# Kernel optimization log

Measured on AMD Instinct MI355X. Metric: run time of the kernel, lower is better.

## Reference

```python
import jax, jax.numpy as jnp
import numpy as np

L, H, DH = 4, 8, 64            # num_layers, num_heads, hidden_dim (= dim_per_head)
HD = H * DH                    # 512 = per-layer q/k/v width
R, BLOCK, NREG, NW = 3, 128, 8, 8   # n_hashes, block_size, num_regions, num_w_per_dist
CDIM, LAT = 2, 3               # coords_dim, latent_dim
SCALE = 1.0 / float(np.sqrt(DH))


def layer_norm(x, g, b):
    m = x.mean(-1, keepdims=True)
    v = ((x - m) ** 2).mean(-1, keepdims=True)
    return (x - m) * jax.lax.rsqrt(v + 1e-5) * g + b


def hept_attention(q, k, v, coords, batch, w_head, hash_proj):
    # HEPT: E2LSH hash + region/batch bucketing -> sort -> blockwise attention
    # with RPE distance bias, combined over hash rounds by logsumexp weights.
    N = q.shape[0]
    nb = N // BLOCK
    qh = q.reshape(N, H, DH)
    kh = k.reshape(N, H, DH)
    vh = v.reshape(N, H, DH)
    c0 = coords[:, 0]
    region = jnp.clip(((c0 - c0.min()) / (c0.max() - c0.min() + 1e-6) * NREG).astype(jnp.int32), 0, NREG - 1)
    c_rpe = coords[:, 1:]                       # [N, CDIM-1] dims used for RPE distances
    bf = batch.astype(jnp.float32)
    outs, lses = [], []
    for r in range(R):
        hv = coords @ hash_proj[r]              # [N] LSH projection
        hn = (hv - hv.min()) / (hv.max() - hv.min() + 1e-6)
        skey = (bf * NREG + region.astype(jnp.float32)) * 2.0 + hn  # batch-major, region, hash
        idx = jnp.argsort(skey)
        inv = jnp.argsort(idx)
        qs = qh[idx].reshape(nb, BLOCK, H, DH)
        ks = kh[idx].reshape(nb, BLOCK, H, DH)
        vs = vh[idx].reshape(nb, BLOCK, H, DH)
        cs = c_rpe[idx].reshape(nb, BLOCK, CDIM - 1)
        bs = batch[idx].reshape(nb, BLOCK)
        scores = jnp.einsum('bihd,bjhd->bhij', qs, ks) * SCALE     # [nb,H,B,B]
        d2 = (cs[:, :, None, :] - cs[:, None, :, :]) ** 2          # [nb,B,B,CDIM-1]
        scores = scores - jnp.einsum('hc,bijc->bhij', w_head, d2)  # RPE distance penalty
        scores = jnp.where((bs[:, :, None] == bs[:, None, :])[:, None], scores, -1e9)
        lse = jax.nn.logsumexp(scores, axis=-1)                    # [nb,H,B]
        p = jnp.exp(scores - lse[..., None])
        o = jnp.einsum('bhij,bjhd->bihd', p, vs).reshape(N, H, DH)
        outs.append(o[inv])
        lses.append(jnp.transpose(lse, (0, 2, 1)).reshape(N, H)[inv])
    wts = jax.nn.softmax(jnp.stack(lses), axis=0)[..., None]       # [R,N,H,1]
    return (wts * jnp.stack(outs)).sum(0).reshape(N, HD)


def _forward(x, coords, batch, enc_W1, enc_b1, enc_W2, enc_b2, ln1_g, ln1_b, wq, wk, wv,
             rpe_W, wo, ln2_g, ln2_b, ff_W1, ff_b1, ff_W2, ff_b2, W_cat,
             mlp_W1, mlp_b1, mlp_W2, mlp_b2, beta_W1, beta_b1, beta_W2, beta_b2,
             coord_W1, coord_b1, coord_W2, coord_b2, hash_proj):
    h0 = jax.nn.relu(x @ enc_W1 + enc_b1) @ enc_W2 + enc_b2
    feats = [h0]
    cur = h0
    for l in range(L):
        xn = layer_norm(cur, ln1_g[l], ln1_b[l])
        q = xn @ wq[l]
        k = xn @ wk[l]
        v = xn @ wv[l]
        # per-head positive RPE weights derived from w_rpe weight matrix
        w_head = jax.nn.softplus(rpe_W[l].reshape(CDIM - 1, NW, H, DH).mean(axis=(1, 3)).T)  # [H,CDIM-1]
        a = hept_attention(q, k, v, coords, batch, w_head, hash_proj) @ wo[l]
        cur = cur + a
        ffo = jax.nn.relu(layer_norm(cur, ln2_g[l], ln2_b[l]) @ ff_W1[l] + ff_b1[l]) @ ff_W2[l] + ff_b2[l]
        cur = cur + ffo
        feats.append(cur)
    enc2 = jnp.concatenate(feats, axis=-1) @ W_cat
    out = enc2 + (jax.nn.relu(enc2 @ mlp_W1 + mlp_b1) @ mlp_W2 + mlp_b2)
    eps = 1e-6
    beta = jnp.clip(jax.nn.sigmoid(jax.nn.relu(out @ beta_W1 + beta_b1) @ beta_W2 + beta_b2), eps, 1.0 - eps)
    hcoord = jax.nn.relu(out @ coord_W1 + coord_b1) @ coord_W2 + coord_b2
    return beta, hcoord


def setup_inputs() -> dict:
    key = jax.random.key(0)
    ks = jax.random.split(key, 40)
    N, IN_DIM = 32768, 16
    def w(i, shape, s=0.05):
        return jax.random.normal(ks[i], shape, jnp.float32) * s
    return dict(
        x=jax.random.normal(ks[0], (N, IN_DIM), jnp.float32),
        coords=jax.random.normal(ks[1], (N, CDIM), jnp.float32),
        batch=jnp.sort(jax.random.randint(ks[2], (N,), 0, 8)),
        enc_W1=w(3, (IN_DIM, DH)), enc_b1=jnp.zeros((DH,), jnp.float32),
        enc_W2=w(4, (DH, DH)), enc_b2=jnp.zeros((DH,), jnp.float32),
        ln1_g=jnp.ones((L, DH), jnp.float32), ln1_b=jnp.zeros((L, DH), jnp.float32),
        wq=w(5, (L, DH, HD)), wk=w(6, (L, DH, HD)), wv=w(7, (L, DH, HD)),
        rpe_W=w(8, (L, NW * (CDIM - 1), HD)),
        wo=w(9, (L, HD, DH)),
        ln2_g=jnp.ones((L, DH), jnp.float32), ln2_b=jnp.zeros((L, DH), jnp.float32),
        ff_W1=w(10, (L, DH, DH)), ff_b1=jnp.zeros((L, DH), jnp.float32),
        ff_W2=w(11, (L, DH, DH)), ff_b2=jnp.zeros((L, DH), jnp.float32),
        W_cat=w(12, (DH * (L + 1), DH // 2)),
        mlp_W1=w(13, (DH // 2, DH // 2)), mlp_b1=jnp.zeros((DH // 2,), jnp.float32),
        mlp_W2=w(14, (DH // 2, DH // 2)), mlp_b2=jnp.zeros((DH // 2,), jnp.float32),
        beta_W1=w(15, (DH // 2, DH // 4)), beta_b1=jnp.zeros((DH // 4,), jnp.float32),
        beta_W2=w(16, (DH // 4, 1)), beta_b2=jnp.zeros((1,), jnp.float32),
        coord_W1=w(17, (DH // 2, DH // 4)), coord_b1=jnp.zeros((DH // 4,), jnp.float32),
        coord_W2=w(18, (DH // 4, LAT)), coord_b2=jnp.zeros((LAT,), jnp.float32),
        hash_proj=jax.random.normal(ks[19], (R, CDIM), jnp.float32),
    )


def reference(x, coords, batch, enc_W1, enc_b1, enc_W2, enc_b2, ln1_g, ln1_b, wq, wk, wv,
              rpe_W, wo, ln2_g, ln2_b, ff_W1, ff_b1, ff_W2, ff_b2, W_cat,
              mlp_W1, mlp_b1, mlp_W2, mlp_b2, beta_W1, beta_b1, beta_W2, beta_b2,
              coord_W1, coord_b1, coord_W2, coord_b2, hash_proj):
    return _forward(x, coords, batch, enc_W1, enc_b1, enc_W2, enc_b2, ln1_g, ln1_b, wq, wk, wv,
                    rpe_W, wo, ln2_g, ln2_b, ff_W1, ff_b1, ff_W2, ff_b2, W_cat,
                    mlp_W1, mlp_b1, mlp_W2, mlp_b2, beta_W1, beta_b1, beta_W2, beta_b2,
                    coord_W1, coord_b1, coord_W2, coord_b2, hash_proj)
```

## Files before the change

kernel.cpp:

```cpp
#include <hip/hip_runtime.h>
#include <math.h>

#define DEV __device__ __forceinline__

constexpr int DHc = 64;
constexpr int HDc = 512;
constexpr int Hc  = 8;
constexpr int BLKc = 128;

typedef float f32x16 __attribute__((ext_vector_type(16)));
typedef short s16x8  __attribute__((ext_vector_type(8)));

union FragU { unsigned u[4]; s16x8 v; };

DEV unsigned fenc(float f){ unsigned u = __float_as_uint(f); return (u & 0x80000000u) ? ~u : (u | 0x80000000u); }
DEV float fdec(unsigned u){ unsigned b = (u & 0x80000000u) ? (u ^ 0x80000000u) : ~u; return __uint_as_float(b); }
DEV float hv_calc(float c0, float c1, float h0, float h1){
  return __fadd_rn(__fmul_rn(c0, h0), __fmul_rn(c1, h1));
}
DEV unsigned short f2bf(float f){
  unsigned u = __float_as_uint(f);
  return (unsigned short)((u + 0x7FFFu + ((u >> 16) & 1u)) >> 16);
}
DEV float bf2f(unsigned short s){ return __uint_as_float((unsigned)s << 16); }

DEV unsigned cvtpk(float lo, float hi){
  unsigned r;
  asm("v_cvt_pk_bf16_f32 %0, %1, %2" : "=v"(r) : "v"(lo), "v"(hi));
  return r;
}
DEV void pswap(unsigned &a, unsigned &b){
  asm volatile("v_permlane32_swap_b32 %0, %1" : "+v"(a), "+v"(b));
}

__global__ void minmax_init_kernel(unsigned* mm){
  int t = threadIdx.x;
  if (t < 4) mm[t] = 0xFFFFFFFFu;
  else if (t < 8) mm[t] = 0u;
}

__global__ void minmax_reduce_kernel(const float* __restrict__ coords, const float* __restrict__ hp,
                                     unsigned* mm, int N)
{
  float h[6];
  #pragma unroll
  for (int i = 0; i < 6; ++i) h[i] = hp[i];
  float mn[4] = {3.0e38f, 3.0e38f, 3.0e38f, 3.0e38f};
  float mx[4] = {-3.0e38f, -3.0e38f, -3.0e38f, -3.0e38f};
  for (int i = blockIdx.x*blockDim.x + threadIdx.x; i < N; i += gridDim.x*blockDim.x){
    float c0 = coords[2*i], c1 = coords[2*i+1];
    float v0 = c0;
    float v1 = hv_calc(c0, c1, h[0], h[1]);
    float v2 = hv_calc(c0, c1, h[2], h[3]);
    float v3 = hv_calc(c0, c1, h[4], h[5]);
    mn[0] = fminf(mn[0], v0); mx[0] = fmaxf(mx[0], v0);
    mn[1] = fminf(mn[1], v1); mx[1] = fmaxf(mx[1], v1);
    mn[2] = fminf(mn[2], v2); mx[2] = fmaxf(mx[2], v2);
    mn[3] = fminf(mn[3], v3); mx[3] = fmaxf(mx[3], v3);
  }
  #pragma unroll
  for (int o = 1; o < 64; o <<= 1){
    #pragma unroll
    for (int s = 0; s < 4; ++s){
      mn[s] = fminf(mn[s], __shfl_xor(mn[s], o));
      mx[s] = fmaxf(mx[s], __shfl_xor(mx[s], o));
    }
  }
  if ((threadIdx.x & 63) == 0){
    #pragma unroll
    for (int s = 0; s < 4; ++s){
      atomicMin(&mm[s],   fenc(mn[s]));
      atomicMax(&mm[4+s], fenc(mx[s]));
    }
  }
}

__global__ void make_keys_kernel(const float* __restrict__ coords, const int* __restrict__ batch,
                                 const float* __restrict__ hp, const unsigned* __restrict__ mm,
                                 unsigned long long* __restrict__ keys, int N)
{
  int i = blockIdx.x*blockDim.x + threadIdx.x;
  if (i >= N) return;
  float c0 = coords[2*i], c1 = coords[2*i+1];
  float c0min = fdec(mm[0]), c0max = fdec(mm[4]);
  float rf = (c0 - c0min) / (c0max - c0min + 1e-6f) * 8.0f;
  int region = (int)rf;
  region = region < 0 ? 0 : (region > 7 ? 7 : region);
  float base2 = ((float)batch[i] * 8.0f + (float)region) * 2.0f;
  #pragma unroll
  for (int r = 0; r < 3; ++r){
    float hv = hv_calc(c0, c1, hp[2*r], hp[2*r+1]);
    float hn = (hv - fdec(mm[1+r])) / (fdec(mm[5+r]) - fdec(mm[1+r]) + 1e-6f);
    float skey = base2 + hn;
    keys[(size_t)r*N + i] = ((unsigned long long)__float_as_uint(skey) << 32) | (unsigned)i;
  }
}

__global__ void bitonic_local_full_kernel(unsigned long long* keys, int N)
{
  __shared__ unsigned long long sh[1024];
  unsigned long long* a = keys + (size_t)blockIdx.y * N;
  int base = blockIdx.x * 1024, t = threadIdx.x;
  sh[t] = a[base + t];
  __syncthreads();
  for (int k = 2; k <= 1024; k <<= 1){
    bool dirup = (((base + t) & k) == 0);
    for (int j = k >> 1; j > 0; j >>= 1){
      int l = t ^ j;
      if (l > t){
        unsigned long long x = sh[t], y = sh[l];
        if ((x > y) == dirup){ sh[t] = y; sh[l] = x; }
      }
      __syncthreads();
    }
  }
  a[base + t] = sh[t];
}

__global__ void bitonic_global_kernel(unsigned long long* keys, int N, int k, int j)
{
  unsigned long long* a = keys + (size_t)blockIdx.y * N;
  int i = blockIdx.x*blockDim.x + threadIdx.x;
  int l = i ^ j;
  if (l > i && l < N){
    unsigned long long x = a[i], y = a[l];
    bool dirup = ((i & k) == 0);
    if ((x > y) == dirup){ a[i] = y; a[l] = x; }
  }
}

__global__ void bitonic_local_merge_kernel(unsigned long long* keys, int N, int k)
{
  __shared__ unsigned long long sh[1024];
  unsigned long long* a = keys + (size_t)blockIdx.y * N;
  int base = blockIdx.x * 1024, t = threadIdx.x;
  sh[t] = a[base + t];
  __syncthreads();
  bool dirup = ((base & k) == 0);
  for (int j = 512; j > 0; j >>= 1){
    int l = t ^ j;
    if (l > t){
      unsigned long long x = sh[t], y = sh[l];
      if ((x > y) == dirup){ sh[t] = y; sh[l] = x; }
    }
    __syncthreads();
  }
  a[base + t] = sh[t];
}

__global__ void extract_idx_kernel(const unsigned long long* __restrict__ keys, int* __restrict__ idx, int total)
{
  int i = blockIdx.x*blockDim.x + threadIdx.x;
  if (i < total) idx[i] = (int)(keys[i] & 0xFFFFFFFFull);
}

__global__ void wconv_kernel(const float* __restrict__ wq, const float* __restrict__ wk,
                             const float* __restrict__ wv, const float* __restrict__ wo,
                             unsigned short* __restrict__ wqkvT, unsigned short* __restrict__ woT)
{
  int tid = blockIdx.x*blockDim.x + threadIdx.x;
  const int NQ = 4*3*512*64;
  if (tid < NQ){
    int kk = tid & 63;
    int rest = tid >> 6;
    int n = rest & 511;
    int rest2 = rest >> 9;
    int z = rest2 % 3, l = rest2 / 3;
    const float* W = (z==0) ? wq : (z==1) ? wk : wv;
    wqkvT[tid] = f2bf(W[((size_t)l*64 + kk)*512 + n]);
  } else if (tid < NQ + 4*64*512){
    int e = tid - NQ;
    int kk = e & 511;
    int rest = e >> 9;
    int n = rest & 63;
    int l = rest >> 6;
    woT[e] = f2bf(wo[((size_t)l*512 + kk)*64 + n]);
  }
}

__global__ __launch_bounds__(256) void encoder_kernel(const float* __restrict__ x,
    const float* __restrict__ W1, const float* __restrict__ b1,
    const float* __restrict__ W2, const float* __restrict__ b2,
    float* __restrict__ h0, int N)
{
  __shared__ float W1s[16][64];
  __shared__ __align__(16) float W2s[64][64];
  __shared__ float xs[4][16];
  __shared__ float t1s[4][64];
  int t = threadIdx.x;
  for (int f = t; f < 1024; f += 256) W1s[f>>6][f&63] = W1[f];
  #pragma unroll
  for (int e = 0; e < 4; ++e){ int f = t + e*256; *(float4*)&W2s[f>>4][(f&15)*4] = *(const float4*)&W2[f*4]; }
  int w = t >> 6, d = t & 63;
  int row = blockIdx.x*4 + w;
  if (d < 16) xs[w][d] = x[(size_t)row*16 + d];
  __syncthreads();
  float acc = b1[d];
  #pragma unroll
  for (int i = 0; i < 16; ++i) acc += xs[w][i]*W1s[i][d];
  t1s[w][d] = fmaxf(acc, 0.f);
  __syncthreads();
  float acc2 = b2[d];
  #pragma unroll
  for (int i = 0; i < 64; ++i) acc2 += t1s[w][i]*W2s[i][d];
  h0[(size_t)row*64 + d] = acc2;
}

__global__ __launch_bounds__(256) void ln_kernel(const float* __restrict__ in,
    const float* __restrict__ g, const float* __restrict__ bln, unsigned short* __restrict__ out, int N)
{
  int t = threadIdx.x, w = t >> 6, d = t & 63;
  int row = blockIdx.x*4 + w;
  float v = in[(size_t)row*64 + d];
  float s = v;
  #pragma unroll
  for (int o = 1; o < 64; o <<= 1) s += __shfl_xor(s, o);
  float mean = s * (1.0f/64.0f);
  float dv = v - mean, sq = dv*dv;
  #pragma unroll
  for (int o = 1; o < 64; o <<= 1) sq += __shfl_xor(sq, o);
  out[(size_t)row*64 + d] = f2bf(dv * rsqrtf(sq*(1.0f/64.0f) + 1e-5f) * g[d] + bln[d]);
}

__global__ __launch_bounds__(256) void qkv_mfma_kernel(
    const unsigned short* __restrict__ xnb, const unsigned short* __restrict__ wqkvT_l,
    unsigned short* __restrict__ q, unsigned short* __restrict__ k, unsigned short* __restrict__ v, int N)
{
  __shared__ __align__(16) unsigned short a_lds[128*64];
  __shared__ __align__(16) unsigned short b_lds[128*64];
  int z = blockIdx.z;
  unsigned short* C = (z==0) ? q : (z==1) ? k : v;
  const unsigned short* wT = wqkvT_l + (size_t)z*512*64;
  int rb = blockIdx.x*128, cb = blockIdx.y*128;
  int t = threadIdx.x;
  #pragma unroll
  for (int e = 0; e < 4; ++e){
    int f = t + e*256; int row = f >> 3, ch = f & 7;
    *(s16x8*)&a_lds[row*64 + ((ch ^ (row&7))*8)] = *(const s16x8*)&xnb[(size_t)(rb+row)*64 + ch*8];
    *(s16x8*)&b_lds[row*64 + ((ch ^ (row&7))*8)] = *(const s16x8*)&wT[(size_t)(cb+row)*64 + ch*8];
  }
  __syncthreads();
  int w = t >> 6, l = t & 63, lo = l & 31, hi = l >> 5;
  s16x8 bf[4];
  #pragma unroll
  for (int ks = 0; ks < 4; ++ks){
    int brow = w*32 + lo, s = (ks<<1)|hi;
    bf[ks] = *(const s16x8*)&b_lds[brow*64 + ((s ^ (brow&7))*8)];
  }
  f32x16 acc[4];
  #pragma unroll
  for (int mt = 0; mt < 4; ++mt)
    #pragma unroll
    for (int i = 0; i < 16; ++i) acc[mt][i] = 0.f;
  #pragma unroll
  for (int mt = 0; mt < 4; ++mt){
    int arow = mt*32 + lo;
    #pragma unroll
    for (int ks = 0; ks < 4; ++ks){
      int s = (ks<<1)|hi;
      s16x8 af = *(const s16x8*)&a_lds[arow*64 + ((s ^ (arow&7))*8)];
      acc[mt] = __builtin_amdgcn_mfma_f32_32x32x16_bf16(af, bf[ks], acc[mt], 0, 0, 0);
    }
  }
  #pragma unroll
  for (int mt = 0; mt < 4; ++mt)
    #pragma unroll
    for (int reg = 0; reg < 16; ++reg){
      int m = mt*32 + (reg&3) + 8*(reg>>2) + 4*hi;
      C[(size_t)(rb+m)*HDc + cb + w*32 + lo] = f2bf(acc[mt][reg]);
    }
}

__global__ void whead_kernel(const float* __restrict__ rpe, float* __restrict__ wh)
{
  int h = blockIdx.x, d = threadIdx.x;
  float s = 0.f;
  #pragma unroll
  for (int w = 0; w < 8; ++w) s += rpe[(size_t)w*512 + h*64 + d];
  #pragma unroll
  for (int o = 1; o < 64; o <<= 1) s += __shfl_xor(s, o);
  if (d == 0){
    float m = s * (1.0f/512.0f);
    wh[h] = fmaxf(m, 0.f) + log1pf(expf(-fabsf(m)));
  }
}

__global__ __launch_bounds__(256, 3) void attn_kernel(
    const unsigned short* __restrict__ qm, const unsigned short* __restrict__ km,
    const unsigned short* __restrict__ vm,
    const float* __restrict__ coords, const int* __restrict__ batch,
    const int* __restrict__ idx_all, const float* __restrict__ w_head,
    float* __restrict__ lse_all, unsigned short* __restrict__ o_buf, int N)
{
  __shared__ __align__(16) unsigned short qlds[128*64];
  __shared__ __align__(16) unsigned short klds[128*64];
  __shared__ __align__(16) unsigned short vtl[64*128];
  __shared__ __align__(16) float c1s[BLKc];
  __shared__ __align__(16) int   bts[BLKc];
  __shared__ int   idxs[BLKc];
  __shared__ __align__(16) float isel[BLKc];
  int b = blockIdx.x, h = blockIdx.y, r = blockIdx.z, t = threadIdx.x;
  const int* idx_r = idx_all + (size_t)r*N;
  if (t < BLKc){
    int g = idx_r[b*BLKc + t];
    idxs[t] = g; c1s[t] = coords[2*g+1]; bts[t] = batch[g];
  }
  __syncthreads();
  #pragma unroll
  for (int e = 0; e < 4; ++e){
    int f = t + e*256;
    int row = f >> 3, ch = f & 7;
    int g = idxs[row];
    s16x8 qv = *(const s16x8*)&qm[(size_t)g*HDc + h*DHc + ch*8];
    s16x8 kv = *(const s16x8*)&km[(size_t)g*HDc + h*DHc + ch*8];
    *(s16x8*)&qlds[row*64 + ((ch ^ (row&7))*8)] = qv;
    *(s16x8*)&klds[row*64 + ((ch ^ (row&7))*8)] = kv;
  }
  #pragma unroll
  for (int e = 0; e < 2; ++e){
    int pf = t + e*256;
    int jp = pf >> 3, dc = pf & 7;
    int j0 = jp*2, j1 = j0+1;
    s16x8 v0 = *(const s16x8*)&vm[(size_t)idxs[j0]*HDc + h*DHc + dc*8];
    s16x8 v1 = *(const s16x8*)&vm[(size_t)idxs[j1]*HDc + h*DHc + dc*8];
    int cj = jp >> 2;
    int jo = jp & 3;
    #pragma unroll
    for (int i = 0; i < 8; ++i){
      int d = dc*8 + i;
      unsigned val = (unsigned)(unsigned short)v0[i] | ((unsigned)(unsigned short)v1[i] << 16);
      *(unsigned*)&vtl[d*128 + ((cj ^ (d&7))*8) + jo*2] = val;
    }
  }
  __syncthreads();

  int w = t >> 6, l = t & 63, lo = l & 31, hi = l >> 5;
  int qrow = w*32 + lo;

  s16x8 qf[4];
  #pragma unroll
  for (int ks = 0; ks < 4; ++ks)
    qf[ks] = *(const s16x8*)&qlds[qrow*64 + ((((ks<<1)|hi) ^ (qrow&7))*8)];

  f32x16 acc[4];
  #pragma unroll
  for (int kt = 0; kt < 4; ++kt)
    #pragma unroll
    for (int i = 0; i < 16; ++i) acc[kt][i] = 0.f;

  #pragma unroll
  for (int kt = 0; kt < 4; ++kt){
    int krow = kt*32 + lo;
    #pragma unroll
    for (int ks = 0; ks < 4; ++ks){
      s16x8 kf = *(const s16x8*)&klds[krow*64 + ((((ks<<1)|hi) ^ (krow&7))*8)];
      acc[kt] = __builtin_amdgcn_mfma_f32_32x32x16_bf16(kf, qf[ks], acc[kt], 0, 0, 0);
    }
  }

  float c1i = c1s[qrow]; int bti = bts[qrow];
  float wh = w_head[h];
  #pragma unroll
  for (int kt = 0; kt < 4; ++kt){
    #pragma unroll
    for (int rq = 0; rq < 4; ++rq){
      int kb = kt*32 + rq*8 + hi*4;
      float4 c4 = *(const float4*)&c1s[kb];
      int4  b4 = *(const int4*)&bts[kb];
      #pragma unroll
      for (int j = 0; j < 4; ++j){
        int reg = rq*4 + j;
        float c1k = (j==0)?c4.x:(j==1)?c4.y:(j==2)?c4.z:c4.w;
        int   btk = (j==0)?b4.x:(j==1)?b4.y:(j==2)?b4.z:b4.w;
        float dd = c1i - c1k;
        float sc = acc[kt][reg]*0.125f - wh*dd*dd;
        if (bti != btk) sc = -1e9f;
        acc[kt][reg] = sc;
      }
    }
  }

  float m = -3.0e38f;
  #pragma unroll
  for (int kt = 0; kt < 4; ++kt)
    #pragma unroll
    for (int i = 0; i < 16; ++i) m = fmaxf(m, acc[kt][i]);
  m = fmaxf(m, __shfl_xor(m, 32));
  float se = 0.f;
  #pragma unroll
  for (int kt = 0; kt < 4; ++kt)
    #pragma unroll
    for (int i = 0; i < 16; ++i){
      float p = __expf(acc[kt][i] - m);
      acc[kt][i] = p;
      se += p;
    }
  se += __shfl_xor(se, 32);
  if (l < 32){
    int gi0 = idxs[qrow];
    lse_all[((size_t)r*N + gi0)*Hc + h] = m + __logf(se);
    isel[qrow] = 1.0f / se;
  }

  f32x16 oa0, oa1;
  #pragma unroll
  for (int i = 0; i < 16; ++i){ oa0[i] = 0.f; oa1[i] = 0.f; }

  #pragma unroll
  for (int kt = 0; kt < 4; ++kt){
    unsigned X = cvtpk(acc[kt][0],  acc[kt][1]);
    unsigned Z = cvtpk(acc[kt][2],  acc[kt][3]);
    unsigned Y = cvtpk(acc[kt][4],  acc[kt][5]);
    unsigned W = cvtpk(acc[kt][6],  acc[kt][7]);
    pswap(X, Y); pswap(Z, W);
    FragU f0; f0.u[0]=X; f0.u[1]=Z; f0.u[2]=Y; f0.u[3]=W;
    unsigned X2 = cvtpk(acc[kt][8],  acc[kt][9]);
    unsigned Z2 = cvtpk(acc[kt][10], acc[kt][11]);
    unsigned Y2 = cvtpk(acc[kt][12], acc[kt][13]);
    unsigned W2 = cvtpk(acc[kt][14], acc[kt][15]);
    pswap(X2, Y2); pswap(Z2, W2);
    FragU f1; f1.u[0]=X2; f1.u[1]=Z2; f1.u[2]=Y2; f1.u[3]=W2;
    #pragma unroll
    for (int hks = 0; hks < 2; ++hks){
      s16x8 pa = hks ? f1.v : f0.v;
      int kch = kt*4 + hks*2 + hi;
      int d0 = lo;
      s16x8 vf0 = *(const s16x8*)&vtl[d0*128 + ((kch ^ (d0&7))*8)];
      oa0 = __builtin_amdgcn_mfma_f32_32x32x16_bf16(pa, vf0, oa0, 0, 0, 0);
      int d1 = 32 + lo;
      s16x8 vf1 = *(const s16x8*)&vtl[d1*128 + ((kch ^ (d1&7))*8)];
      oa1 = __builtin_amdgcn_mfma_f32_32x32x16_bf16(pa, vf1, oa1, 0, 0, 0);
    }
  }

  unsigned short* orow = o_buf + (size_t)r*N*HDc;
  #pragma unroll
  for (int rq = 0; rq < 4; ++rq){
    float4 s4 = *(const float4*)&isel[w*32 + rq*8 + hi*4];
    #pragma unroll
    for (int j = 0; j < 4; ++j){
      int reg = rq*4 + j;
      int qq = rq*8 + hi*4 + j;
      int g = idxs[w*32 + qq];
      float sv = (j==0)?s4.x:(j==1)?s4.y:(j==2)?s4.z:s4.w;
      unsigned short* dst = &orow[(size_t)g*HDc + h*DHc + lo];
      dst[0]  = f2bf(oa0[reg]*sv);
      dst[32] = f2bf(oa1[reg]*sv);
    }
  }
}

__global__ __launch_bounds__(256) void wo_mfma_kernel(
    const unsigned short* __restrict__ o_buf, const float* __restrict__ lse_all,
    const unsigned short* __restrict__ woT_l, float* __restrict__ cur, int N)
{
  __shared__ __align__(16) unsigned short As[64*128];
  __shared__ __align__(16) unsigned short Bs[64*128];
  __shared__ float wts[64][24];
  int rb = blockIdx.x*64, t = threadIdx.x;
  #pragma unroll
  for (int e = 0; e < 2; ++e){
    int p = t + e*256;
    int rr = p >> 3, h = p & 7;
    float l0 = lse_all[((size_t)0*N + rb+rr)*Hc + h];
    float l1 = lse_all[((size_t)1*N + rb+rr)*Hc + h];
    float l2 = lse_all[((size_t)2*N + rb+rr)*Hc + h];
    float lm = fmaxf(l0, fmaxf(l1, l2));
    float e0 = __expf(l0-lm), e1 = __expf(l1-lm), e2 = __expf(l2-lm);
    float inv = 1.0f/(e0+e1+e2);
    wts[rr][h*3+0] = e0*inv; wts[rr][h*3+1] = e1*inv; wts[rr][h*3+2] = e2*inv;
  }
  int w = t >> 6, l = t & 63, lo = l & 31, hi = l >> 5;
  int mt = w >> 1, nt = w & 1;
  f32x16 acc;
  #pragma unroll
  for (int i = 0; i < 16; ++i) acc[i] = 0.f;
  for (int kt = 0; kt < 4; ++kt){
    __syncthreads();
    #pragma unroll
    for (int e = 0; e < 4; ++e){
      int f = t + e*256; int rr = f >> 4, kc = f & 15;
      int k0 = kt*128 + kc*8;
      int h = k0 >> 6;
      float w0 = wts[rr][h*3+0], w1 = wts[rr][h*3+1], w2 = wts[rr][h*3+2];
      s16x8 u0 = *(const s16x8*)&o_buf[((size_t)0*N + rb+rr)*HDc + k0];
      s16x8 u1 = *(const s16x8*)&o_buf[((size_t)1*N + rb+rr)*HDc + k0];
      s16x8 u2 = *(const s16x8*)&o_buf[((size_t)2*N + rb+rr)*HDc + k0];
      FragU fo;
      #pragma unroll
      for (int ii = 0; ii < 4; ++ii){
        float a0 = w0*bf2f((unsigned short)u0[2*ii])   + w1*bf2f((unsigned short)u1[2*ii])   + w2*bf2f((unsigned short)u2[2*ii]);
        float a1 = w0*bf2f((unsigned short)u0[2*ii+1]) + w1*bf2f((unsigned short)u1[2*ii+1]) + w2*bf2f((unsigned short)u2[2*ii+1]);
        fo.u[ii] = cvtpk(a0, a1);
      }
      *(s16x8*)&As[rr*128 + ((kc ^ (rr&7))*8)] = fo.v;
      *(s16x8*)&Bs[rr*128 + ((kc ^ (rr&7))*8)] = *(const s16x8*)&woT_l[(size_t)rr*512 + k0];
    }
    __syncthreads();
    #pragma unroll
    for (int ks = 0; ks < 8; ++ks){
      int s = ks*2 + hi;
      int arow = mt*32 + lo, brow = nt*32 + lo;
      s16x8 af = *(const s16x8*)&As[arow*128 + ((s ^ (arow&7))*8)];
      s16x8 bfr = *(const s16x8*)&Bs[brow*128 + ((s ^ (brow&7))*8)];
      acc = __builtin_amdgcn_mfma_f32_32x32x16_bf16(af, bfr, acc, 0, 0, 0);
    }
  }
  #pragma unroll
  for (int reg = 0; reg < 16; ++reg){
    int m = mt*32 + (reg&3) + 8*(reg>>2) + 4*hi;
    int n = nt*32 + lo;
    cur[(size_t)(rb+m)*64 + n] += acc[reg];
  }
}

__global__ __launch_bounds__(256) void ffn_kernel(float* __restrict__ cur,
    const float* __restrict__ g, const float* __restrict__ bln,
    const float* __restrict__ W1, const float* __restrict__ b1,
    const float* __restrict__ W2, const float* __restrict__ b2, int N)
{
  __shared__ __align__(16) float W1s[64][64];
  __shared__ __align__(16) float W2s[64][64];
  __shared__ float xns[4][64];
  __shared__ float t1s[4][64];
  int t = threadIdx.x;
  #pragma unroll
  for (int e = 0; e < 4; ++e){
    int f = t + e*256; int rr = f >> 4, c4 = f & 15;
    *(float4*)&W1s[rr][c4*4] = *(const float4*)&W1[f*4];
    *(float4*)&W2s[rr][c4*4] = *(const float4*)&W2[f*4];
  }
  int w = t >> 6, d = t & 63;
  int row = blockIdx.x*4 + w;
  float v = cur[(size_t)row*64 + d];
  float s = v;
  #pragma unroll
  for (int o = 1; o < 64; o <<= 1) s += __shfl_xor(s, o);
  float mean = s * (1.0f/64.0f);
  float dv = v - mean, sq = dv*dv;
  #pragma unroll
  for (int o = 1; o < 64; o <<= 1) sq += __shfl_xor(sq, o);
  float xnv = dv * rsqrtf(sq*(1.0f/64.0f) + 1e-5f) * g[d] + bln[d];
  xns[w][d] = xnv;
  __syncthreads();
  float acc = b1[d];
  #pragma unroll
  for (int i = 0; i < 64; ++i) acc += xns[w][i]*W1s[i][d];
  t1s[w][d] = fmaxf(acc, 0.f);
  __syncthreads();
  float acc2 = b2[d];
  #pragma unroll
  for (int i = 0; i < 64; ++i) acc2 += t1s[w][i]*W2s[i][d];
  cur[(size_t)row*64 + d] = v + acc2;
}

__global__ __launch_bounds__(256) void enc2_accum_kernel(const float* __restrict__ cur,
    const float* __restrict__ Wcat, float* __restrict__ enc2, int rowoff, int store, int N)
{
  __shared__ float Ws[64][32];
  __shared__ float crs[8][64];
  int t = threadIdx.x;
  for (int f = t; f < 2048; f += 256) Ws[f>>5][f&31] = Wcat[(size_t)(rowoff + (f>>5))*32 + (f&31)];
  for (int f = t; f < 512; f += 256) crs[f>>6][f&63] = cur[(size_t)(blockIdx.x*8 + (f>>6))*64 + (f&63)];
  __syncthreads();
  int r8 = t >> 5, c = t & 31;
  int row = blockIdx.x*8 + r8;
  float acc = 0.f;
  #pragma unroll
  for (int d = 0; d < 64; ++d) acc += crs[r8][d]*Ws[d][c];
  size_t o = (size_t)row*32 + c;
  if (store) enc2[o] = acc; else enc2[o] += acc;
}

__global__ __launch_bounds__(256) void head_kernel(const float* __restrict__ enc2,
    const float* mW1, const float* mb1, const float* mW2, const float* mb2,
    const float* bW1, const float* bb1, const float* bW2, const float* bb2,
    const float* cW1, const float* cb1, const float* cW2, const float* cb2,
    float* __restrict__ outp, int N)
{
  __shared__ float s_mW1[32][32], s_mW2[32][32], s_bW1[32][16], s_cW1[32][16];
  __shared__ float s_bW2[16], s_cW2[16][3];
  __shared__ float e2[8][32], t1[8][32], ov[8][32], bt[8][16], ct[8][16];
  int t = threadIdx.x;
  for (int f = t; f < 1024; f += 256){ s_mW1[f>>5][f&31] = mW1[f]; s_mW2[f>>5][f&31] = mW2[f]; }
  for (int f = t; f < 512; f += 256){ s_bW1[f>>4][f&15] = bW1[f]; s_cW1[f>>4][f&15] = cW1[f]; }
  if (t < 16) s_bW2[t] = bW2[t];
  if (t < 48) s_cW2[t/3][t%3] = cW2[t];
  int r8 = t >> 5, c = t & 31;
  int row = blockIdx.x*8 + r8;
  float e = enc2[(size_t)row*32 + c];
  e2[r8][c] = e;
  __syncthreads();
  float a = mb1[c];
  #pragma unroll
  for (int i = 0; i < 32; ++i) a += e2[r8][i]*s_mW1[i][c];
  t1[r8][c] = fmaxf(a, 0.f);
  __syncthreads();
  float o = e + mb2[c];
  #pragma unroll
  for (int i = 0; i < 32; ++i) o += t1[r8][i]*s_mW2[i][c];
  ov[r8][c] = o;
  __syncthreads();
  if (c < 16){
    float a2 = bb1[c];
    #pragma unroll
    for (int i = 0; i < 32; ++i) a2 += ov[r8][i]*s_bW1[i][c];
    bt[r8][c] = fmaxf(a2, 0.f);
  } else {
    int cc = c - 16;
    float a2 = cb1[cc];
    #pragma unroll
    for (int i = 0; i < 32; ++i) a2 += ov[r8][i]*s_cW1[i][cc];
    ct[r8][cc] = fmaxf(a2, 0.f);
  }
  __syncthreads();
  if (c == 0){
    float a3 = bb2[0];
    #pragma unroll
    for (int i = 0; i < 16; ++i) a3 += bt[r8][i]*s_bW2[i];
    float sg = 1.0f / (1.0f + __expf(-a3));
    sg = fminf(fmaxf(sg, 1e-6f), 1.0f - 1e-6f);
    outp[row] = sg;
  } else if (c < 4){
    int dd = c - 1;
    float a3 = cb2[dd];
    #pragma unroll
    for (int i = 0; i < 16; ++i) a3 += ct[r8][i]*s_cW2[i][dd];
    outp[(size_t)N + (size_t)row*3 + dd] = a3;
  }
}

extern "C" void kernel_launch(void* const* d_in, const int* in_sizes, int n_in,
                              void* d_out, int out_size, void* d_ws, size_t ws_size,
                              hipStream_t stream)
{
  const float* x       = (const float*)d_in[0];
  const float* coords  = (const float*)d_in[1];
  const int*   batch   = (const int*)d_in[2];
  const float* enc_W1  = (const float*)d_in[3];
  const float* enc_b1  = (const float*)d_in[4];
  const float* enc_W2  = (const float*)d_in[5];
  const float* enc_b2  = (const float*)d_in[6];
  const float* ln1_g   = (const float*)d_in[7];
  const float* ln1_b   = (const float*)d_in[8];
  const float* wq      = (const float*)d_in[9];
  const float* wk      = (const float*)d_in[10];
  const float* wv      = (const float*)d_in[11];
  const float* rpe_W   = (const float*)d_in[12];
  const float* wo      = (const float*)d_in[13];
  const float* ln2_g   = (const float*)d_in[14];
  const float* ln2_b   = (const float*)d_in[15];
  const float* ff_W1   = (const float*)d_in[16];
  const float* ff_b1   = (const float*)d_in[17];
  const float* ff_W2   = (const float*)d_in[18];
  const float* ff_b2   = (const float*)d_in[19];
  const float* W_cat   = (const float*)d_in[20];
  const float* mlp_W1  = (const float*)d_in[21];
  const float* mlp_b1  = (const float*)d_in[22];
  const float* mlp_W2  = (const float*)d_in[23];
  const float* mlp_b2  = (const float*)d_in[24];
  const float* beta_W1 = (const float*)d_in[25];
  const float* beta_b1 = (const float*)d_in[26];
  const float* beta_W2 = (const float*)d_in[27];
  const float* beta_b2 = (const float*)d_in[28];
  const float* coord_W1= (const float*)d_in[29];
  const float* coord_b1= (const float*)d_in[30];
  const float* coord_W2= (const float*)d_in[31];
  const float* coord_b2= (const float*)d_in[32];
  const float* hash_proj=(const float*)d_in[33];

  const int N  = in_sizes[0] / 16;
  const int nb = N / 128;
  float* outp = (float*)d_out;
  (void)out_size; (void)ws_size; (void)n_in;

  char* p = (char*)d_ws;
  size_t off = 0;
  auto alloc = [&](size_t bytes) -> char* {
    char* r = p + off;
    off += (bytes + 255) & ~(size_t)255;
    return r;
  };
  float* cur    = (float*)alloc((size_t)N*64*4);
  unsigned short* xnb = (unsigned short*)alloc((size_t)N*64*2);
  unsigned short* q = (unsigned short*)alloc((size_t)N*512*2);
  unsigned short* k = (unsigned short*)alloc((size_t)N*512*2);
  unsigned short* v = (unsigned short*)alloc((size_t)N*512*2);
  unsigned short* o_buf = (unsigned short*)alloc((size_t)3*N*512*2);
  float* enc2   = (float*)alloc((size_t)N*32*4);
  float* lse    = (float*)alloc((size_t)3*N*8*4);
  unsigned long long* keys = (unsigned long long*)alloc((size_t)3*N*8);
  int* idx      = (int*)alloc((size_t)3*N*4);
  unsigned short* wqkvT = (unsigned short*)alloc((size_t)4*3*512*64*2);
  unsigned short* woT   = (unsigned short*)alloc((size_t)4*64*512*2);
  unsigned* mm  = (unsigned*)alloc(256);
  float* whead  = (float*)alloc(256);

  wconv_kernel<<<2048, 256, 0, stream>>>(wq, wk, wv, wo, wqkvT, woT);

  minmax_init_kernel<<<1, 64, 0, stream>>>(mm);
  minmax_reduce_kernel<<<256, 256, 0, stream>>>(coords, hash_proj, mm, N);
  make_keys_kernel<<<(N+255)/256, 256, 0, stream>>>(coords, batch, hash_proj, mm, keys, N);
  bitonic_local_full_kernel<<<dim3(N/1024, 3), 1024, 0, stream>>>(keys, N);
  for (int kk = 2048; kk <= N; kk <<= 1){
    for (int j = kk >> 1; j >= 1024; j >>= 1)
      bitonic_global_kernel<<<dim3(N/256, 3), 256, 0, stream>>>(keys, N, kk, j);
    bitonic_local_merge_kernel<<<dim3(N/1024, 3), 1024, 0, stream>>>(keys, N, kk);
  }
  extract_idx_kernel<<<(3*N+255)/256, 256, 0, stream>>>(keys, idx, 3*N);

  encoder_kernel<<<N/4, 256, 0, stream>>>(x, enc_W1, enc_b1, enc_W2, enc_b2, cur, N);
  enc2_accum_kernel<<<N/8, 256, 0, stream>>>(cur, W_cat, enc2, 0, 1, N);

  for (int l = 0; l < 4; ++l){
    ln_kernel<<<N/4, 256, 0, stream>>>(cur, ln1_g + l*64, ln1_b + l*64, xnb, N);
    qkv_mfma_kernel<<<dim3(N/128, 4, 3), 256, 0, stream>>>(xnb,
        wqkvT + (size_t)l*3*512*64, q, k, v, N);
    whead_kernel<<<8, 64, 0, stream>>>(rpe_W + (size_t)l*8*512, whead);
    attn_kernel<<<dim3(nb, 8, 3), 256, 0, stream>>>(q, k, v, coords, batch,
        idx, whead, lse, o_buf, N);
    wo_mfma_kernel<<<N/64, 256, 0, stream>>>(o_buf, lse, woT + (size_t)l*64*512, cur, N);
    ffn_kernel<<<N/4, 256, 0, stream>>>(cur, ln2_g + l*64, ln2_b + l*64,
        ff_W1 + (size_t)l*64*64, ff_b1 + l*64, ff_W2 + (size_t)l*64*64, ff_b2 + l*64, N);
    enc2_accum_kernel<<<N/8, 256, 0, stream>>>(cur, W_cat, enc2, (l+1)*64, 0, N);
  }

  head_kernel<<<N/8, 256, 0, stream>>>(enc2, mlp_W1, mlp_b1, mlp_W2, mlp_b2,
      beta_W1, beta_b1, beta_W2, beta_b2, coord_W1, coord_b1, coord_W2, coord_b2, outp, N);
}
```

Before: 906.7 us.

## Fuse layernorm into encoder/FFN, widen bitonic sort tiles, batch whead, misc tweaks

Folds the pre-attention layernorm into the encoder and FFN epilogues, which removes a separate LN kernel launch and its round trip through memory each layer. Bitonic sort local stages now work on 2048-element tiles, so fewer global merge passes run. The whead computation for all layers moves out of the loop into one launch, and the 1/sqrt(d) scale is folded into the Q projection. Other changes: an attention fast path that skips the batch mask when a block holds a single batch id, setprio around the MFMA loops, a block-level reduction before atomics in minmax, and 32-row tiles in enc2_accum. Together these add code complexity, and the bf16 rounding of Q now happens after scaling rather than before.

```diff
diff --git a/kernel.cpp b/kernel.cpp
--- a/kernel.cpp
+++ b/kernel.cpp
@@ -39,20 +39,21 @@
   else if (t < 8) mm[t] = 0u;
 }
 
-__global__ void minmax_reduce_kernel(const float* __restrict__ coords, const float* __restrict__ hp,
-                                     unsigned* mm, int N)
-{
+__global__ __launch_bounds__(256) void minmax_reduce_kernel(const float* __restrict__ coords,
+    const float* __restrict__ hp, unsigned* mm, int N)
+{
+  __shared__ float red[4][8];
   float h[6];
   #pragma unroll
   for (int i = 0; i < 6; ++i) h[i] = hp[i];
   float mn[4] = {3.0e38f, 3.0e38f, 3.0e38f, 3.0e38f};
   float mx[4] = {-3.0e38f, -3.0e38f, -3.0e38f, -3.0e38f};
   for (int i = blockIdx.x*blockDim.x + threadIdx.x; i < N; i += gridDim.x*blockDim.x){
-    float c0 = coords[2*i], c1 = coords[2*i+1];
-    float v0 = c0;
-    float v1 = hv_calc(c0, c1, h[0], h[1]);
-    float v2 = hv_calc(c0, c1, h[2], h[3]);
-    float v3 = hv_calc(c0, c1, h[4], h[5]);
+    float2 c = *(const float2*)&coords[2*i];
+    float v0 = c.x;
+    float v1 = hv_calc(c.x, c.y, h[0], h[1]);
+    float v2 = hv_calc(c.x, c.y, h[2], h[3]);
+    float v3 = hv_calc(c.x, c.y, h[4], h[5]);
     mn[0] = fminf(mn[0], v0); mx[0] = fmaxf(mx[0], v0);
     mn[1] = fminf(mn[1], v1); mx[1] = fmaxf(mx[1], v1);
     mn[2] = fminf(mn[2], v2); mx[2] = fmaxf(mx[2], v2);
@@ -66,12 +67,19 @@
       mx[s] = fmaxf(mx[s], __shfl_xor(mx[s], o));
     }
   }
+  int w = threadIdx.x >> 6;
   if ((threadIdx.x & 63) == 0){
     #pragma unroll
-    for (int s = 0; s < 4; ++s){
-      atomicMin(&mm[s],   fenc(mn[s]));
-      atomicMax(&mm[4+s], fenc(mx[s]));
-    }
+    for (int s = 0; s < 4; ++s){ red[w][s] = mn[s]; red[w][4+s] = mx[s]; }
+  }
+  __syncthreads();
+  int t = threadIdx.x;
+  if (t < 4){
+    float v = fminf(fminf(red[0][t], red[1][t]), fminf(red[2][t], red[3][t]));
+    atomicMin(&mm[t], fenc(v));
+  } else if (t < 8){
+    float v = fmaxf(fmaxf(red[0][t], red[1][t]), fmaxf(red[2][t], red[3][t]));
+    atomicMax(&mm[t], fenc(v));
   }
 }
 
@@ -96,25 +104,25 @@
   }
 }
 
-__global__ void bitonic_local_full_kernel(unsigned long long* keys, int N)
-{
-  __shared__ unsigned long long sh[1024];
+__global__ __launch_bounds__(1024) void bitonic_local_full2k_kernel(unsigned long long* keys, int N)
+{
+  __shared__ unsigned long long sh[2048];
   unsigned long long* a = keys + (size_t)blockIdx.y * N;
-  int base = blockIdx.x * 1024, t = threadIdx.x;
+  int base = blockIdx.x * 2048, t = threadIdx.x;
   sh[t] = a[base + t];
-  __syncthreads();
-  for (int k = 2; k <= 1024; k <<= 1){
-    bool dirup = (((base + t) & k) == 0);
+  sh[t + 1024] = a[base + t + 1024];
+  __syncthreads();
+  for (int k = 2; k <= 2048; k <<= 1){
     for (int j = k >> 1; j > 0; j >>= 1){
-      int l = t ^ j;
-      if (l > t){
-        unsigned long long x = sh[t], y = sh[l];
-        if ((x > y) == dirup){ sh[t] = y; sh[l] = x; }
-      }
+      int i = ((t & ~(j-1)) << 1) | (t & (j-1));
+      bool dirup = (((base + i) & k) == 0);
+      unsigned long long x = sh[i], y = sh[i+j];
+      if ((x > y) == dirup){ sh[i] = y; sh[i+j] = x; }
       __syncthreads();
     }
   }
   a[base + t] = sh[t];
+  a[base + t + 1024] = sh[t + 1024];
 }
 
 __global__ void bitonic_global_kernel(unsigned long long* keys, int N, int k, int j)
@@ -129,23 +137,23 @@
   }
 }
 
-__global__ void bitonic_local_merge_kernel(unsigned long long* keys, int N, int k)
-{
-  __shared__ unsigned long long sh[1024];
+__global__ __launch_bounds__(1024) void bitonic_local_merge2k_kernel(unsigned long long* keys, int N, int k)
+{
+  __shared__ unsigned long long sh[2048];
   unsigned long long* a = keys + (size_t)blockIdx.y * N;
-  int base = blockIdx.x * 1024, t = threadIdx.x;
+  int base = blockIdx.x * 2048, t = threadIdx.x;
   sh[t] = a[base + t];
-  __syncthreads();
-  bool dirup = ((base & k) == 0);
-  for (int j = 512; j > 0; j >>= 1){
-    int l = t ^ j;
-    if (l > t){
-      unsigned long long x = sh[t], y = sh[l];
-      if ((x > y) == dirup){ sh[t] = y; sh[l] = x; }
-    }
+  sh[t + 1024] = a[base + t + 1024];
+  __syncthreads();
+  for (int j = 1024; j > 0; j >>= 1){
+    int i = ((t & ~(j-1)) << 1) | (t & (j-1));
+    bool dirup = (((base + i) & k) == 0);
+    unsigned long long x = sh[i], y = sh[i+j];
+    if ((x > y) == dirup){ sh[i] = y; sh[i+j] = x; }
     __syncthreads();
   }
   a[base + t] = sh[t];
+  a[base + t + 1024] = sh[t + 1024];
 }
 
 __global__ void extract_idx_kernel(const unsigned long long* __restrict__ keys, int* __restrict__ idx, int total)
@@ -181,7 +189,8 @@
 __global__ __launch_bounds__(256) void encoder_kernel(const float* __restrict__ x,
     const float* __restrict__ W1, const float* __restrict__ b1,
     const float* __restrict__ W2, const float* __restrict__ b2,
-    float* __restrict__ h0, int N)
+    const float* __restrict__ lng, const float* __restrict__ lnb,
+    float* __restrict__ h0, unsigned short* __restrict__ xnb, int N)
 {
   __shared__ float W1s[16][64];
   __shared__ __align__(16) float W2s[64][64];
@@ -204,22 +213,14 @@
   #pragma unroll
   for (int i = 0; i < 64; ++i) acc2 += t1s[w][i]*W2s[i][d];
   h0[(size_t)row*64 + d] = acc2;
-}
-
-__global__ __launch_bounds__(256) void ln_kernel(const float* __restrict__ in,
-    const float* __restrict__ g, const float* __restrict__ bln, unsigned short* __restrict__ out, int N)
-{
-  int t = threadIdx.x, w = t >> 6, d = t & 63;
-  int row = blockIdx.x*4 + w;
-  float v = in[(size_t)row*64 + d];
-  float s = v;
+  float s = acc2;
   #pragma unroll
   for (int o = 1; o < 64; o <<= 1) s += __shfl_xor(s, o);
   float mean = s * (1.0f/64.0f);
-  float dv = v - mean, sq = dv*dv;
+  float dv = acc2 - mean, sq = dv*dv;
   #pragma unroll
   for (int o = 1; o < 64; o <<= 1) sq += __shfl_xor(sq, o);
-  out[(size_t)row*64 + d] = f2bf(dv * rsqrtf(sq*(1.0f/64.0f) + 1e-5f) * g[d] + bln[d]);
+  xnb[(size_t)row*64 + d] = f2bf(dv * rsqrtf(sq*(1.0f/64.0f) + 1e-5f) * lng[d] + lnb[d]);
 }
 
 __global__ __launch_bounds__(256) void qkv_mfma_kernel(
@@ -231,6 +232,7 @@
   int z = blockIdx.z;
   unsigned short* C = (z==0) ? q : (z==1) ? k : v;
   const unsigned short* wT = wqkvT_l + (size_t)z*512*64;
+  float oscale = (z==0) ? 0.125f : 1.0f;
   int rb = blockIdx.x*128, cb = blockIdx.y*128;
   int t = threadIdx.x;
   #pragma unroll
@@ -267,21 +269,22 @@
     #pragma unroll
     for (int reg = 0; reg < 16; ++reg){
       int m = mt*32 + (reg&3) + 8*(reg>>2) + 4*hi;
-      C[(size_t)(rb+m)*HDc + cb + w*32 + lo] = f2bf(acc[mt][reg]);
+      C[(size_t)(rb+m)*HDc + cb + w*32 + lo] = f2bf(acc[mt][reg]*oscale);
     }
 }
 
 __global__ void whead_kernel(const float* __restrict__ rpe, float* __restrict__ wh)
 {
-  int h = blockIdx.x, d = threadIdx.x;
+  int l = blockIdx.x >> 3, h = blockIdx.x & 7, d = threadIdx.x;
+  const float* rp = rpe + (size_t)l*8*512;
   float s = 0.f;
   #pragma unroll
-  for (int w = 0; w < 8; ++w) s += rpe[(size_t)w*512 + h*64 + d];
+  for (int w = 0; w < 8; ++w) s += rp[(size_t)w*512 + h*64 + d];
   #pragma unroll
   for (int o = 1; o < 64; o <<= 1) s += __shfl_xor(s, o);
   if (d == 0){
     float m = s * (1.0f/512.0f);
-    wh[h] = fmaxf(m, 0.f) + log1pf(expf(-fabsf(m)));
+    wh[blockIdx.x] = fmaxf(m, 0.f) + log1pf(expf(-fabsf(m)));
   }
 }
 
@@ -299,6 +302,7 @@
   __shared__ __align__(16) int   bts[BLKc];
   __shared__ int   idxs[BLKc];
   __shared__ __align__(16) float isel[BLKc];
+  __shared__ int unif;
   int b = blockIdx.x, h = blockIdx.y, r = blockIdx.z, t = threadIdx.x;
   const int* idx_r = idx_all + (size_t)r*N;
   if (t < BLKc){
@@ -306,6 +310,7 @@
     idxs[t] = g; c1s[t] = coords[2*g+1]; bts[t] = batch[g];
   }
   __syncthreads();
+  if (t == 0) unif = (bts[0] == bts[127]);
   #pragma unroll
   for (int e = 0; e < 4; ++e){
     int f = t + e*256;
@@ -348,6 +353,7 @@
     #pragma unroll
     for (int i = 0; i < 16; ++i) acc[kt][i] = 0.f;
 
+  __builtin_amdgcn_s_setprio(1);
   #pragma unroll
   for (int kt = 0; kt < 4; ++kt){
     int krow = kt*32 + lo;
@@ -357,9 +363,11 @@
       acc[kt] = __builtin_amdgcn_mfma_f32_32x32x16_bf16(kf, qf[ks], acc[kt], 0, 0, 0);
     }
   }
+  __builtin_amdgcn_s_setprio(0);
 
   float c1i = c1s[qrow]; int bti = bts[qrow];
   float wh = w_head[h];
+  int msk = unif;
   #pragma unroll
   for (int kt = 0; kt < 4; ++kt){
     #pragma unroll
@@ -373,8 +381,8 @@
         float c1k = (j==0)?c4.x:(j==1)?c4.y:(j==2)?c4.z:c4.w;
         int   btk = (j==0)?b4.x:(j==1)?b4.y:(j==2)?b4.z:b4.w;
         float dd = c1i - c1k;
-        float sc = acc[kt][reg]*0.125f - wh*dd*dd;
-        if (bti != btk) sc = -1e9f;
+        float sc = acc[kt][reg] - wh*dd*dd;
+        if (!msk && bti != btk) sc = -1e9f;
         acc[kt][reg] = sc;
       }
     }
@@ -406,6 +414,7 @@
   #pragma unroll
   for (int i = 0; i < 16; ++i){ oa0[i] = 0.f; oa1[i] = 0.f; }
 
+  __builtin_amdgcn_s_setprio(1);
   #pragma unroll
   for (int kt = 0; kt < 4; ++kt){
     unsigned X = cvtpk(acc[kt][0],  acc[kt][1]);
@@ -432,6 +441,7 @@
       oa1 = __builtin_amdgcn_mfma_f32_32x32x16_bf16(pa, vf1, oa1, 0, 0, 0);
     }
   }
+  __builtin_amdgcn_s_setprio(0);
 
   unsigned short* orow = o_buf + (size_t)r*N*HDc;
   #pragma unroll
@@ -517,7 +527,9 @@
 __global__ __launch_bounds__(256) void ffn_kernel(float* __restrict__ cur,
     const float* __restrict__ g, const float* __restrict__ bln,
     const float* __restrict__ W1, const float* __restrict__ b1,
-    const float* __restrict__ W2, const float* __restrict__ b2, int N)
+    const float* __restrict__ W2, const float* __restrict__ b2,
+    const float* __restrict__ nlg, const float* __restrict__ nlb,
+    unsigned short* __restrict__ xnb, int N)
 {
   __shared__ __align__(16) float W1s[64][64];
   __shared__ __align__(16) float W2s[64][64];
@@ -551,25 +563,38 @@
   float acc2 = b2[d];
   #pragma unroll
   for (int i = 0; i < 64; ++i) acc2 += t1s[w][i]*W2s[i][d];
-  cur[(size_t)row*64 + d] = v + acc2;
+  float nv = v + acc2;
+  cur[(size_t)row*64 + d] = nv;
+  if (nlg){
+    float s2 = nv;
+    #pragma unroll
+    for (int o = 1; o < 64; o <<= 1) s2 += __shfl_xor(s2, o);
+    float mean2 = s2 * (1.0f/64.0f);
+    float dv2 = nv - mean2, sq2 = dv2*dv2;
+    #pragma unroll
+    for (int o = 1; o < 64; o <<= 1) sq2 += __shfl_xor(sq2, o);
+    xnb[(size_t)row*64 + d] = f2bf(dv2 * rsqrtf(sq2*(1.0f/64.0f) + 1e-5f) * nlg[d] + nlb[d]);
+  }
 }
 
 __global__ __launch_bounds__(256) void enc2_accum_kernel(const float* __restrict__ cur,
     const float* __restrict__ Wcat, float* __restrict__ enc2, int rowoff, int store, int N)
 {
-  __shared__ float Ws[64][32];
-  __shared__ float crs[8][64];
+  __shared__ float Ws[64][33];
+  __shared__ float crs[32][65];
   int t = threadIdx.x;
   for (int f = t; f < 2048; f += 256) Ws[f>>5][f&31] = Wcat[(size_t)(rowoff + (f>>5))*32 + (f&31)];
-  for (int f = t; f < 512; f += 256) crs[f>>6][f&63] = cur[(size_t)(blockIdx.x*8 + (f>>6))*64 + (f&63)];
+  for (int f = t; f < 2048; f += 256) crs[f>>6][f&63] = cur[(size_t)(blockIdx.x*32 + (f>>6))*64 + (f&63)];
   __syncthreads();
   int r8 = t >> 5, c = t & 31;
-  int row = blockIdx.x*8 + r8;
-  float acc = 0.f;
-  #pragma unroll
-  for (int d = 0; d < 64; ++d) acc += crs[r8][d]*Ws[d][c];
-  size_t o = (size_t)row*32 + c;
-  if (store) enc2[o] = acc; else enc2[o] += acc;
+  for (int rr = r8; rr < 32; rr += 8){
+    int row = blockIdx.x*32 + rr;
+    float acc = 0.f;
+    #pragma unroll
+    for (int d = 0; d < 64; ++d) acc += crs[rr][d]*Ws[d][c];
+    size_t o = (size_t)row*32 + c;
+    if (store) enc2[o] = acc; else enc2[o] += acc;
+  }
 }
 
 __global__ __launch_bounds__(256) void head_kernel(const float* __restrict__ enc2,
@@ -697,32 +722,35 @@
   float* whead  = (float*)alloc(256);
 
   wconv_kernel<<<2048, 256, 0, stream>>>(wq, wk, wv, wo, wqkvT, woT);
+  whead_kernel<<<32, 64, 0, stream>>>(rpe_W, whead);
 
   minmax_init_kernel<<<1, 64, 0, stream>>>(mm);
-  minmax_reduce_kernel<<<256, 256, 0, stream>>>(coords, hash_proj, mm, N);
+  minmax_reduce_kernel<<<64, 256, 0, stream>>>(coords, hash_proj, mm, N);
   make_keys_kernel<<<(N+255)/256, 256, 0, stream>>>(coords, batch, hash_proj, mm, keys, N);
-  bitonic_local_full_kernel<<<dim3(N/1024, 3), 1024, 0, stream>>>(keys, N);
-  for (int kk = 2048; kk <= N; kk <<= 1){
-    for (int j = kk >> 1; j >= 1024; j >>= 1)
+  bitonic_local_full2k_kernel<<<dim3(N/2048, 3), 1024, 0, stream>>>(keys, N);
+  for (int kk = 4096; kk <= N; kk <<= 1){
+    for (int j = kk >> 1; j >= 2048; j >>= 1)
       bitonic_global_kernel<<<dim3(N/256, 3), 256, 0, stream>>>(keys, N, kk, j);
-    bitonic_local_merge_kernel<<<dim3(N/1024, 3), 1024, 0, stream>>>(keys, N, kk);
+    bitonic_local_merge2k_kernel<<<dim3(N/2048, 3), 1024, 0, stream>>>(keys, N, kk);
   }
   extract_idx_kernel<<<(3*N+255)/256, 256, 0, stream>>>(keys, idx, 3*N);
 
-  encoder_kernel<<<N/4, 256, 0, stream>>>(x, enc_W1, enc_b1, enc_W2, enc_b2, cur, N);
-  enc2_accum_kernel<<<N/8, 256, 0, stream>>>(cur, W_cat, enc2, 0, 1, N);
+  encoder_kernel<<<N/4, 256, 0, stream>>>(x, enc_W1, enc_b1, enc_W2, enc_b2,
+      ln1_g, ln1_b, cur, xnb, N);
+  enc2_accum_kernel<<<N/32, 256, 0, stream>>>(cur, W_cat, enc2, 0, 1, N);
 
   for (int l = 0; l < 4; ++l){
-    ln_kernel<<<N/4, 256, 0, stream>>>(cur, ln1_g + l*64, ln1_b + l*64, xnb, N);
     qkv_mfma_kernel<<<dim3(N/128, 4, 3), 256, 0, stream>>>(xnb,
         wqkvT + (size_t)l*3*512*64, q, k, v, N);
-    whead_kernel<<<8, 64, 0, stream>>>(rpe_W + (size_t)l*8*512, whead);
     attn_kernel<<<dim3(nb, 8, 3), 256, 0, stream>>>(q, k, v, coords, batch,
-        idx, whead, lse, o_buf, N);
+        idx, whead + l*8, lse, o_buf, N);
     wo_mfma_kernel<<<N/64, 256, 0, stream>>>(o_buf, lse, woT + (size_t)l*64*512, cur, N);
+    const float* nlg = (l < 3) ? (ln1_g + (l+1)*64) : nullptr;
+    const float* nlb = (l < 3) ? (ln1_b + (l+1)*64) : nullptr;
     ffn_kernel<<<N/4, 256, 0, stream>>>(cur, ln2_g + l*64, ln2_b + l*64,
-        ff_W1 + (size_t)l*64*64, ff_b1 + l*64, ff_W2 + (size_t)l*64*64, ff_b2 + l*64, N);
-    enc2_accum_kernel<<<N/8, 256, 0, stream>>>(cur, W_cat, enc2, (l+1)*64, 0, N);
+        ff_W1 + (size_t)l*64*64, ff_b1 + l*64, ff_W2 + (size_t)l*64*64, ff_b2 + l*64,
+        nlg, nlb, xnb, N);
+    enc2_accum_kernel<<<N/32, 256, 0, stream>>>(cur, W_cat, enc2, (l+1)*64, 0, N);
   }
 
   head_kernel<<<N/8, 256, 0, stream>>>(enc2, mlp_W1, mlp_b1, mlp_W2, mlp_b2,
```

New measurement: 800.4 us. -11.7%, faster.
